# Kernel optimization log

Measured on AMD Instinct MI355X. Metric: run time of the kernel, lower is better.

The kernel has to match this reference:

```python
import jax, jax.numpy as jnp
import numpy as np

NUM_POINTS = 16384
OVERSAMPLE = 3
IMPORTANCE_RATIO = 0.75


def point_sample(feat, coords):
    """grid_sample(bilinear, align_corners=False, zero padding) at [0,1]^2 coords.
    feat: (N, C, H, W); coords: (N, P, 2) with coords[...,0]=x (width), [...,1]=y.
    Returns (N, C, P)."""
    N, C, H, W = feat.shape
    # grid_sample with g = 2c-1, align_corners=False -> pixel = c*size - 0.5
    x = coords[..., 0] * W - 0.5
    y = coords[..., 1] * H - 0.5
    x0 = jnp.floor(x)
    y0 = jnp.floor(y)
    x1 = x0 + 1.0
    y1 = y0 + 1.0
    wx1 = x - x0
    wx0 = 1.0 - wx1
    wy1 = y - y0
    wy0 = 1.0 - wy1
    featf = feat.reshape(N, C, H * W)

    def gather(yi, xi):
        valid = (xi >= 0) & (xi <= W - 1) & (yi >= 0) & (yi <= H - 1)
        xic = jnp.clip(xi, 0, W - 1).astype(jnp.int32)
        yic = jnp.clip(yi, 0, H - 1).astype(jnp.int32)
        idx = yic * W + xic  # (N, P)
        v = jnp.take_along_axis(featf, idx[:, None, :], axis=2)  # (N, C, P)
        return v * valid[:, None, :].astype(feat.dtype)

    out = (gather(y0, x0) * (wy0 * wx0)[:, None, :]
           + gather(y0, x1) * (wy0 * wx1)[:, None, :]
           + gather(y1, x0) * (wy1 * wx0)[:, None, :]
           + gather(y1, x1) * (wy1 * wx1)[:, None, :])
    return out


def calculate_uncertainty(logits):
    """logits: (N, C, P) -> (N, P) uncertainty = top2 - top1 (<= 0)."""
    if logits.shape[1] == 1:
        return -jnp.abs(logits)[:, 0, :]
    top2 = jax.lax.top_k(jnp.moveaxis(logits, 1, -1), 2)[0]  # (N, P, 2)
    return top2[..., 1] - top2[..., 0]


def sample_point_coords(coarse_logits):
    """get_uncertain_point_coords_with_randomness (torch.no_grad branch)."""
    N = coarse_logits.shape[0]
    num_sampled = NUM_POINTS * OVERSAMPLE
    num_imp = int(IMPORTANCE_RATIO * NUM_POINTS)
    num_rand = NUM_POINTS - num_imp
    k1, k2 = jax.random.split(jax.random.key(7))
    cand = jax.random.uniform(k1, (N, num_sampled, 2), dtype=jnp.float32)
    cand_logits = point_sample(coarse_logits, cand)  # (N, C, S)
    unc = calculate_uncertainty(cand_logits)  # (N, S)
    idx = jax.lax.top_k(unc, num_imp)[1]  # (N, num_imp)
    imp = jnp.take_along_axis(cand, idx[..., None], axis=1)  # (N, num_imp, 2)
    rand = jax.random.uniform(k2, (N, num_rand, 2), dtype=jnp.float32)
    return jnp.concatenate([imp, rand], axis=1)  # (N, P, 2)


def point_head(fine, coarse_pts, w0, b0, w1, b1, w2, b2, wp, bp):
    x = jnp.concatenate([fine, coarse_pts], axis=1)  # (N, nin+C, P)
    for w, b in ((w0, b0), (w1, b1), (w2, b2)):
        x = jax.nn.relu(jnp.einsum('oc,ncp->nop', w, x) + b[None, :, None])
        x = jnp.concatenate([x, coarse_pts], axis=1)  # coarse_pred_each_layer
    return jnp.einsum('oc,ncp->nop', wp, x) + bp[None, :, None]  # (N, C, P)


def setup_inputs() -> dict:
    key = jax.random.key(0)
    ks = jax.random.split(key, 8)
    N, C, Hc, Wc = 8, 19, 64, 64
    nin, Hf, Wf = 256, 128, 128
    fin = nin + C  # 275
    return {
        'coarse_sem_seg_logits': jax.random.normal(ks[0], (N, C, Hc, Wc), jnp.float32),
        'features': jax.random.normal(ks[1], (N, nin, Hf, Wf), jnp.float32),
        'w0': jax.random.normal(ks[2], (nin, fin), jnp.float32) * (2.0 / fin) ** 0.5,
        'b0': jnp.zeros((nin,), jnp.float32),
        'w1': jax.random.normal(ks[3], (nin, fin), jnp.float32) * (2.0 / fin) ** 0.5,
        'b1': jnp.zeros((nin,), jnp.float32),
        'w2': jax.random.normal(ks[4], (nin, fin), jnp.float32) * (2.0 / fin) ** 0.5,
        'b2': jnp.zeros((nin,), jnp.float32),
        'wp': jax.random.normal(ks[5], (C, fin), jnp.float32) * 0.001,
        'bp': jnp.zeros((C,), jnp.float32),
    }


def reference(coarse_sem_seg_logits, features, w0, b0, w1, b1, w2, b2, wp, bp):
    # training-mode forward of PointRendSemSegHead
    point_coords = jax.lax.stop_gradient(
        sample_point_coords(jax.lax.stop_gradient(coarse_sem_seg_logits)))
    coarse_pts = point_sample(coarse_sem_seg_logits, point_coords)  # (N, C, P)
    fine_pts = point_sample(features, point_coords)  # (N, nin, P)
    point_logits = point_head(fine_pts, coarse_pts, w0, b0, w1, b1, w2, b2, wp, bp)
    return coarse_sem_seg_logits, point_logits, point_coords
```

## Files before the change

### kernel.cpp

```cpp
#include <hip/hip_runtime.h>
#include <stdint.h>

#pragma clang fp contract(off)

#define NB    8
#define CCH   19
#define FCH   256
#define FIN   275
#define KP    288
#define NPTS  16384
#define NSAMP 49152
#define NIMP  12288
#define NRAND 4096
#define SORT_M 65536
#define CHUNK  8192
#define TP    64
#define XROW  640
#define WBF_OFF (4u << 20)
#define FTR_OFF (8u << 20)
#define FTR_BYTES (134217728ull / 2)

typedef __attribute__((ext_vector_type(8))) short bf16x8;
typedef __attribute__((ext_vector_type(4))) float f32x4;

__host__ __device__ __forceinline__ uint32_t rotl32(uint32_t v, int r) {
  return (v << r) | (v >> (32 - r));
}

__host__ __device__ __forceinline__ void tf2x32(uint32_t k0, uint32_t k1,
                                                uint32_t x0, uint32_t x1,
                                                uint32_t* o0, uint32_t* o1) {
  const uint32_t ks2 = k0 ^ k1 ^ 0x1BD11BDAu;
  x0 += k0; x1 += k1;
#define TF_R(r) { x0 += x1; x1 = rotl32(x1, (r)); x1 ^= x0; }
  TF_R(13) TF_R(15) TF_R(26) TF_R(6)
  x0 += k1;  x1 += ks2 + 1u;
  TF_R(17) TF_R(29) TF_R(16) TF_R(24)
  x0 += ks2; x1 += k0 + 2u;
  TF_R(13) TF_R(15) TF_R(26) TF_R(6)
  x0 += k0;  x1 += k1 + 3u;
  TF_R(17) TF_R(29) TF_R(16) TF_R(24)
  x0 += k1;  x1 += ks2 + 4u;
  TF_R(13) TF_R(15) TF_R(26) TF_R(6)
  x0 += ks2; x1 += k0 + 5u;
#undef TF_R
  *o0 = x0; *o1 = x1;
}

__device__ __forceinline__ float u01_at(uint32_t k0, uint32_t k1, uint32_t i) {
  uint32_t o0, o1;
  tf2x32(k0, k1, 0u, i, &o0, &o1);
  const uint32_t b = o0 ^ o1;
  const float f = __uint_as_float((b >> 9) | 0x3f800000u) - 1.0f;
  return fmaxf(0.0f, f);
}

__device__ __forceinline__ unsigned short f2bf(float f) {
  const uint32_t u = __float_as_uint(f);
  return (unsigned short)((u + 0x7fffu + ((u >> 16) & 1u)) >> 16);
}

__device__ __forceinline__ float bf2f(unsigned short h) {
  return __uint_as_float((uint32_t)h << 16);
}

template <int SZ>
__device__ __forceinline__ void interp(float cx, float cy, int* off, float* wgt) {
  const float X = cx * (float)SZ - 0.5f, Y = cy * (float)SZ - 0.5f;
  const float x0f = floorf(X), y0f = floorf(Y);
  const float fx = X - x0f, fy = Y - y0f;
  const float wx0 = 1.0f - fx, wy0 = 1.0f - fy;
  const int x0 = (int)x0f, y0 = (int)y0f;
  const int x0c = min(max(x0, 0), SZ - 1), x1c = min(max(x0 + 1, 0), SZ - 1);
  const int y0c = min(max(y0, 0), SZ - 1), y1c = min(max(y0 + 1, 0), SZ - 1);
  const bool vx0 = (x0 >= 0) & (x0 <= SZ - 1), vx1 = (x0 >= -1) & (x0 <= SZ - 2);
  const bool vy0 = (y0 >= 0) & (y0 <= SZ - 1), vy1 = (y0 >= -1) & (y0 <= SZ - 2);
  off[0] = y0c * SZ + x0c; wgt[0] = (vy0 & vx0) ? wy0 * wx0 : 0.0f;
  off[1] = y0c * SZ + x1c; wgt[1] = (vy0 & vx1) ? wy0 * fx  : 0.0f;
  off[2] = y1c * SZ + x0c; wgt[2] = (vy1 & vx0) ? fy  * wx0 : 0.0f;
  off[3] = y1c * SZ + x1c; wgt[3] = (vy1 & vx1) ? fy  * fx  : 0.0f;
}

__global__ __launch_bounds__(256) void fusedA(
    const float* __restrict__ feats, unsigned short* __restrict__ ftr,
    const float* __restrict__ coarse, unsigned long long* __restrict__ keys,
    const float* __restrict__ w0, const float* __restrict__ w1,
    const float* __restrict__ w2, const float* __restrict__ wpw,
    unsigned short* __restrict__ wbf, unsigned short* __restrict__ wpb,
    uint32_t k1a, uint32_t k1b, int use_tr) {
  __shared__ unsigned short tile[64][66];
  const int bid = blockIdx.x;
  const int t = threadIdx.x;

  if (bid < 8192) {
    if (!use_tr) return;
    const int nn = bid >> 10;
    const int ct = (bid >> 8) & 3;
    const int pt = bid & 255;
    const int c0 = ct * 64, p0 = pt * 64;
    const float* src = feats + ((size_t)nn << 22);
#pragma unroll 4
    for (int k = 0; k < 16; ++k) {
      const int c = 4 * k + (t >> 6);
      const int p = t & 63;
      tile[p][c] = f2bf(src[((size_t)(c0 + c) << 14) + p0 + p]);
    }
    __syncthreads();
    const int p = t >> 2, q = t & 3;
    const int cb = q * 16;
    uint32_t w[8];
#pragma unroll
    for (int m = 0; m < 8; ++m)
      w[m] = (uint32_t)tile[p][cb + 2 * m] | ((uint32_t)tile[p][cb + 2 * m + 1] << 16);
    unsigned short* dst = ftr + ((((size_t)nn << 14) + p0 + p) << 8) + c0 + cb;
    *(uint4*)(dst)     = make_uint4(w[0], w[1], w[2], w[3]);
    *(uint4*)(dst + 8) = make_uint4(w[4], w[5], w[6], w[7]);
  } else if (bid < 10240) {
    const int tid = (bid - 8192) * 256 + t;
    const int nn = tid >> 16, s = tid & (SORT_M - 1);
    if (s >= NSAMP) { keys[tid] = 0xFFFFFFFFFFFFFFFFull; return; }
    const uint32_t ci = (uint32_t)(((unsigned)nn * NSAMP + (unsigned)s) * 2);
    const float cx = u01_at(k1a, k1b, ci);
    const float cy = u01_at(k1a, k1b, ci + 1);
    const float X = cx * 64.0f - 0.5f, Y = cy * 64.0f - 0.5f;
    const float x0f = floorf(X), y0f = floorf(Y);
    const float fx = X - x0f, fy = Y - y0f;
    const float wx0 = 1.0f - fx, wy0 = 1.0f - fy;
    const int x0 = (int)x0f, y0 = (int)y0f;
    const int x0c = min(max(x0, 0), 63), x1c = min(max(x0 + 1, 0), 63);
    const int y0c = min(max(y0, 0), 63), y1c = min(max(y0 + 1, 0), 63);
    const bool vx0 = (x0 >= 0) & (x0 <= 63), vx1 = (x0 >= -1) & (x0 <= 62);
    const bool vy0 = (y0 >= 0) & (y0 <= 63), vy1 = (y0 >= -1) & (y0 <= 62);
    const float w00 = (vy0 & vx0) ? wy0 * wx0 : 0.0f;
    const float w01 = (vy0 & vx1) ? wy0 * fx  : 0.0f;
    const float w10 = (vy1 & vx0) ? fy  * wx0 : 0.0f;
    const float w11 = (vy1 & vx1) ? fy  * fx  : 0.0f;
    const int o00 = y0c * 64 + x0c, o01 = y0c * 64 + x1c;
    const int o10 = y1c * 64 + x0c, o11 = y1c * 64 + x1c;
    const float* cb = coarse + (size_t)nn * (CCH * 4096);
    float m1 = -3.402823466e38f, m2 = -3.402823466e38f;
    for (int c = 0; c < CCH; ++c) {
      const float* pch = cb + (size_t)c * 4096;
      const float v = ((pch[o00] * w00 + pch[o01] * w01) + pch[o10] * w10) + pch[o11] * w11;
      if (v > m1) { m2 = m1; m1 = v; } else if (v > m2) { m2 = v; }
    }
    const float unc = m2 - m1;
    const uint32_t b = __float_as_uint(unc);
    const uint32_t asc = (b & 0x80000000u) ? ~b : (b | 0x80000000u);
    keys[tid] = ((unsigned long long)(~asc) << 32) | (uint32_t)s;
  } else {
    const int i = (bid - 10240) * 256 + t;
    if (i < 3 * 256 * KP) {
      const int L = i / (256 * KP);
      const int rem = i - L * (256 * KP);
      const int o = rem / KP, k = rem - o * KP;
      const float* W = (L == 0) ? w0 : (L == 1) ? w1 : w2;
      wbf[i] = (k < FIN) ? f2bf(W[o * FIN + k]) : (unsigned short)0;
    } else {
      const int j = i - 3 * 256 * KP;
      const int o = j / KP, k = j - o * KP;
      wpb[j] = (o < CCH && k < FIN) ? f2bf(wpw[o * FIN + k]) : (unsigned short)0;
    }
  }
}

__global__ __launch_bounds__(1024) void bitonic_local(unsigned long long* __restrict__ keys) {
  __shared__ unsigned long long s[CHUNK];
  const int cb = blockIdx.x;
  unsigned long long* a = keys + (size_t)cb * CHUNK;
  const unsigned gbase = (unsigned)(cb * CHUNK) & (SORT_M - 1);
  for (int i = threadIdx.x; i < CHUNK; i += 1024) s[i] = a[i];
  __syncthreads();
  for (int k = 2; k <= CHUNK; k <<= 1) {
    for (int j = k >> 1; j > 0; j >>= 1) {
      for (int pid = threadIdx.x; pid < CHUNK / 2; pid += 1024) {
        const int i = ((pid & ~(j - 1)) << 1) | (pid & (j - 1));
        const int l = i | j;
        const bool up = (((gbase + i) & k) == 0);
        const unsigned long long x = s[i], y = s[l];
        if ((x > y) == up) { s[i] = y; s[l] = x; }
      }
      __syncthreads();
    }
  }
  for (int i = threadIdx.x; i < CHUNK; i += 1024) a[i] = s[i];
}

__global__ __launch_bounds__(256) void bitonic_global(unsigned long long* __restrict__ keys,
                                                      int k, int j) {
  const int t = blockIdx.x * blockDim.x + threadIdx.x;
  const int b = t >> 15, pid = t & 32767;
  const int i = ((pid & ~(j - 1)) << 1) | (pid & (j - 1));
  const int l = i | j;
  const bool up = ((i & k) == 0);
  unsigned long long* a = keys + ((size_t)b << 16);
  const unsigned long long x = a[i], y = a[l];
  if ((x > y) == up) { a[i] = y; a[l] = x; }
}

__global__ __launch_bounds__(1024) void bitonic_finish(unsigned long long* __restrict__ keys,
                                                       int k) {
  __shared__ unsigned long long s[CHUNK];
  const int cb = blockIdx.x;
  unsigned long long* a = keys + (size_t)cb * CHUNK;
  const unsigned gi0 = (unsigned)(cb * CHUNK) & (SORT_M - 1);
  for (int i = threadIdx.x; i < CHUNK; i += 1024) s[i] = a[i];
  __syncthreads();
  const bool up = ((gi0 & k) == 0);
  for (int j = CHUNK >> 1; j > 0; j >>= 1) {
    for (int pid = threadIdx.x; pid < CHUNK / 2; pid += 1024) {
      const int i = ((pid & ~(j - 1)) << 1) | (pid & (j - 1));
      const int l = i | j;
      const unsigned long long x = s[i], y = s[l];
      if ((x > y) == up) { s[i] = y; s[l] = x; }
    }
    __syncthreads();
  }
  for (int i = threadIdx.x; i < CHUNK; i += 1024) a[i] = s[i];
}

__global__ __launch_bounds__(256) void write_coords(const unsigned long long* __restrict__ keys,
                                                    float* __restrict__ outc,
                                                    uint32_t k1a, uint32_t k1b,
                                                    uint32_t k2a, uint32_t k2b) {
  const int t = blockIdx.x * blockDim.x + threadIdx.x;
  if (t >= NB * NPTS) return;
  const int nn = t >> 14, p = t & (NPTS - 1);
  float cx, cy;
  if (p < NIMP) {
    const unsigned idx = (unsigned)(keys[((size_t)nn << 16) + p] & 0xFFFFFFFFu);
    const uint32_t ci = ((unsigned)nn * NSAMP + idx) * 2;
    cx = u01_at(k1a, k1b, ci);
    cy = u01_at(k1a, k1b, ci + 1);
  } else {
    const uint32_t ri = ((unsigned)nn * NRAND + (unsigned)(p - NIMP)) * 2;
    cx = u01_at(k2a, k2b, ri);
    cy = u01_at(k2a, k2b, ri + 1);
  }
  outc[(size_t)t * 2] = cx;
  outc[(size_t)t * 2 + 1] = cy;
}

template <int USE_TR>
__global__ __launch_bounds__(512, 6) void fused_mfma(
    const float* __restrict__ coarse, const float* __restrict__ feats,
    const unsigned short* __restrict__ ftr,
    const float* __restrict__ b0, const float* __restrict__ b1,
    const float* __restrict__ b2, const float* __restrict__ bp,
    const unsigned short* __restrict__ wbf, const unsigned short* __restrict__ wpb,
    const float* __restrict__ pc, float* __restrict__ outl) {
  __shared__ __align__(16) unsigned short xp[TP * (XROW / 2)];

  const int t = threadIdx.x;
  const int nn = blockIdx.x >> 8;
  const int pbase = (blockIdx.x & 255) * TP;

  int offF[4]; float wgtF[4];
  int offC[4]; float wgtC[4];
  int offFc[4]; float wgtFc[4];
  {
    const float2 c = *(const float2*)(pc + ((size_t)nn * NPTS + pbase + (t >> 3)) * 2);
    interp<128>(c.x, c.y, offF, wgtF);
  }
  {
    const float2 c = *(const float2*)(pc + ((size_t)nn * NPTS + pbase + (t & 63)) * 2);
    interp<64>(c.x, c.y, offC, wgtC);
    if (!USE_TR) interp<128>(c.x, c.y, offFc, wgtFc);
  }

  if (USE_TR) {
    const int p = t >> 3, q = t & 7;
    const unsigned short* base = ftr + (((size_t)nn << 14) << 8) + q * 32;
    const unsigned short* n0 = base + ((size_t)offF[0] << 8);
    const unsigned short* n1 = base + ((size_t)offF[1] << 8);
    const unsigned short* n2 = base + ((size_t)offF[2] << 8);
    const unsigned short* n3 = base + ((size_t)offF[3] << 8);
    const float g0 = wgtF[0], g1 = wgtF[1], g2 = wgtF[2], g3 = wgtF[3];
    const unsigned swzp = (unsigned)(p & 7) << 4;
#pragma unroll
    for (int m = 0; m < 4; ++m) {
      const bf16x8 a = *(const bf16x8*)(n0 + m * 8);
      const bf16x8 bq = *(const bf16x8*)(n1 + m * 8);
      const bf16x8 c = *(const bf16x8*)(n2 + m * 8);
      const bf16x8 d = *(const bf16x8*)(n3 + m * 8);
      uint32_t u[4];
#pragma unroll
      for (int e = 0; e < 4; ++e) {
        float v0 = fmaf(bf2f((unsigned short)a[2 * e]), g0,
                   fmaf(bf2f((unsigned short)bq[2 * e]), g1,
                   fmaf(bf2f((unsigned short)c[2 * e]), g2,
                        bf2f((unsigned short)d[2 * e]) * g3)));
        float v1 = fmaf(bf2f((unsigned short)a[2 * e + 1]), g0,
                   fmaf(bf2f((unsigned short)bq[2 * e + 1]), g1,
                   fmaf(bf2f((unsigned short)c[2 * e + 1]), g2,
                        bf2f((unsigned short)d[2 * e + 1]) * g3)));
        u[e] = (uint32_t)f2bf(v0) | ((uint32_t)f2bf(v1) << 16);
      }
      *(uint4*)((char*)xp + p * XROW + (((unsigned)((q * 32 + m * 8) * 2)) ^ swzp)) =
          make_uint4(u[0], u[1], u[2], u[3]);
    }
  }

  for (int i = (USE_TR ? 8192 : 0) + t; i < (KP / 2) * TP; i += 512) {
    const int p = i & (TP - 1);
    const int c0 = (i >> 6) * 2;
    float v0 = 0.0f, v1 = 0.0f;
    if (!USE_TR && c0 < FCH) {
      const float* fb0 = feats + ((size_t)nn << 22) + ((size_t)c0 << 14);
      const float* fb1 = fb0 + 16384;
      v0 = ((fb0[offFc[0]] * wgtFc[0] + fb0[offFc[1]] * wgtFc[1])
           + fb0[offFc[2]] * wgtFc[2]) + fb0[offFc[3]] * wgtFc[3];
      v1 = ((fb1[offFc[0]] * wgtFc[0] + fb1[offFc[1]] * wgtFc[1])
           + fb1[offFc[2]] * wgtFc[2]) + fb1[offFc[3]] * wgtFc[3];
    } else if (c0 >= FCH && c0 < FIN) {
      const float* cb0 = coarse + (size_t)nn * (CCH * 4096) + (size_t)(c0 - FCH) * 4096;
      v0 = ((cb0[offC[0]] * wgtC[0] + cb0[offC[1]] * wgtC[1])
           + cb0[offC[2]] * wgtC[2]) + cb0[offC[3]] * wgtC[3];
      if (c0 + 1 < FIN) {
        const float* cb1 = cb0 + 4096;
        v1 = ((cb1[offC[0]] * wgtC[0] + cb1[offC[1]] * wgtC[1])
             + cb1[offC[2]] * wgtC[2]) + cb1[offC[3]] * wgtC[3];
      }
    }
    const uint32_t u = (uint32_t)f2bf(v0) | ((uint32_t)f2bf(v1) << 16);
    *(uint32_t*)((char*)xp + p * XROW + (((unsigned)(c0 * 2)) ^ ((unsigned)(p & 7) << 4))) = u;
  }

  const int lane = t & 63, wave = t >> 6;
  const int wm = wave & 3, wn = wave >> 2;
  const int l15 = lane & 15, g = lane >> 4;
  const unsigned swz = (unsigned)(l15 & 7) << 4;
  const char* xpB = (const char*)xp;

  const float* Bs[3] = {b0, b1, b2};

  for (int L = 0; L < 3; ++L) {
    __syncthreads();
    const unsigned short* wL = wbf + (size_t)L * (256 * KP);
    const unsigned short* wbase = wL + (size_t)(wm * 64 + l15) * KP + g * 8;

    f32x4 acc[4][2];
#pragma unroll
    for (int mt = 0; mt < 4; ++mt)
#pragma unroll
      for (int nt = 0; nt < 2; ++nt) acc[mt][nt] = (f32x4)(0.0f);

    for (int ks = 0; ks < 9; ++ks) {
      const bf16x8 a0 = *(const bf16x8*)(wbase + 0 * 16 * KP + ks * 32);
      const bf16x8 a1 = *(const bf16x8*)(wbase + 1 * 16 * KP + ks * 32);
      const bf16x8 a2 = *(const bf16x8*)(wbase + 2 * 16 * KP + ks * 32);
      const bf16x8 a3 = *(const bf16x8*)(wbase + 3 * 16 * KP + ks * 32);
      const unsigned kb = (unsigned)(ks * 64 + g * 16) ^ swz;
      const bf16x8 q0 = *(const bf16x8*)(xpB + (wn * 32 + 0 + l15) * XROW + kb);
      const bf16x8 q1 = *(const bf16x8*)(xpB + (wn * 32 + 16 + l15) * XROW + kb);
      acc[0][0] = __builtin_amdgcn_mfma_f32_16x16x32_bf16(a0, q0, acc[0][0], 0, 0, 0);
      acc[1][0] = __builtin_amdgcn_mfma_f32_16x16x32_bf16(a1, q0, acc[1][0], 0, 0, 0);
      acc[2][0] = __builtin_amdgcn_mfma_f32_16x16x32_bf16(a2, q0, acc[2][0], 0, 0, 0);
      acc[3][0] = __builtin_amdgcn_mfma_f32_16x16x32_bf16(a3, q0, acc[3][0], 0, 0, 0);
      acc[0][1] = __builtin_amdgcn_mfma_f32_16x16x32_bf16(a0, q1, acc[0][1], 0, 0, 0);
      acc[1][1] = __builtin_amdgcn_mfma_f32_16x16x32_bf16(a1, q1, acc[1][1], 0, 0, 0);
      acc[2][1] = __builtin_amdgcn_mfma_f32_16x16x32_bf16(a2, q1, acc[2][1], 0, 0, 0);
      acc[3][1] = __builtin_amdgcn_mfma_f32_16x16x32_bf16(a3, q1, acc[3][1], 0, 0, 0);
    }
    __syncthreads();

    const float* __restrict__ Bv = Bs[L];
#pragma unroll
    for (int mt = 0; mt < 4; ++mt) {
      const int ch0 = wm * 64 + mt * 16 + (g << 2);
      const float4 bv = *(const float4*)(Bv + ch0);
#pragma unroll
      for (int nt = 0; nt < 2; ++nt) {
        const int p = wn * 32 + nt * 16 + l15;
        const f32x4 v = acc[mt][nt];
        const unsigned short h0 = f2bf(fmaxf(v[0] + bv.x, 0.0f));
        const unsigned short h1 = f2bf(fmaxf(v[1] + bv.y, 0.0f));
        const unsigned short h2 = f2bf(fmaxf(v[2] + bv.z, 0.0f));
        const unsigned short h3 = f2bf(fmaxf(v[3] + bv.w, 0.0f));
        uint2 u;
        u.x = (uint32_t)h0 | ((uint32_t)h1 << 16);
        u.y = (uint32_t)h2 | ((uint32_t)h3 << 16);
        *(uint2*)((char*)xp + p * XROW + (((unsigned)(ch0 * 2)) ^ swz)) = u;
      }
    }
  }
  __syncthreads();

  const int hmt = wave >> 2, hnt = wave & 3;
  const unsigned short* hbase = wpb + (size_t)(hmt * 16 + l15) * KP + g * 8;
  f32x4 hacc = (f32x4)(0.0f);
  for (int ks = 0; ks < 9; ++ks) {
    const unsigned kb = (unsigned)(ks * 64 + g * 16) ^ swz;
    const bf16x8 ha = *(const bf16x8*)(hbase + ks * 32);
    const bf16x8 hb = *(const bf16x8*)(xpB + (hnt * 16 + l15) * XROW + kb);
    hacc = __builtin_amdgcn_mfma_f32_16x16x32_bf16(ha, hb, hacc, 0, 0, 0);
  }
  const int p = pbase + hnt * 16 + l15;
#pragma unroll
  for (int j = 0; j < 4; ++j) {
    const int ch = hmt * 16 + (g << 2) + j;
    if (ch < CCH)
      outl[((size_t)nn * CCH + ch) * NPTS + p] = hacc[j] + bp[ch];
  }
}

extern "C" void kernel_launch(void* const* d_in, const int* in_sizes, int n_in,
                              void* d_out, int out_size, void* d_ws, size_t ws_size,
                              hipStream_t stream) {
  const float* coarse = (const float*)d_in[0];
  const float* feats  = (const float*)d_in[1];
  const float* w0 = (const float*)d_in[2]; const float* b0 = (const float*)d_in[3];
  const float* w1 = (const float*)d_in[4]; const float* b1 = (const float*)d_in[5];
  const float* w2 = (const float*)d_in[6]; const float* b2 = (const float*)d_in[7];
  const float* wp = (const float*)d_in[8]; const float* bp = (const float*)d_in[9];

  float* out0 = (float*)d_out;
  float* outL = out0 + 622592;
  float* outC = outL + 2490368;

  unsigned long long* keys = (unsigned long long*)d_ws;
  unsigned short* wbf = (unsigned short*)((char*)d_ws + WBF_OFF);
  unsigned short* wpb = wbf + 3 * 256 * KP;
  unsigned short* ftr = (unsigned short*)((char*)d_ws + FTR_OFF);
  const int use_tr = (ws_size >= (size_t)FTR_OFF + FTR_BYTES) ? 1 : 0;

  uint32_t k1a, k1b, k2a, k2b;
  tf2x32(0u, 7u, 0u, 0u, &k1a, &k1b);
  tf2x32(0u, 7u, 0u, 1u, &k2a, &k2b);

  hipMemcpyAsync(out0, coarse, 622592 * sizeof(float),
                 hipMemcpyDeviceToDevice, stream);

  fusedA<<<11140, 256, 0, stream>>>(feats, ftr, coarse, keys,
                                    w0, w1, w2, wp, wbf, wpb, k1a, k1b, use_tr);

  bitonic_local<<<64, 1024, 0, stream>>>(keys);
  bitonic_global<<<1024, 256, 0, stream>>>(keys, 16384, 8192);
  bitonic_finish<<<64, 1024, 0, stream>>>(keys, 16384);
  bitonic_global<<<1024, 256, 0, stream>>>(keys, 32768, 16384);
  bitonic_global<<<1024, 256, 0, stream>>>(keys, 32768, 8192);
  bitonic_finish<<<64, 1024, 0, stream>>>(keys, 32768);
  bitonic_global<<<1024, 256, 0, stream>>>(keys, 65536, 32768);
  bitonic_global<<<1024, 256, 0, stream>>>(keys, 65536, 16384);
  bitonic_global<<<1024, 256, 0, stream>>>(keys, 65536, 8192);
  bitonic_finish<<<64, 1024, 0, stream>>>(keys, 65536);

  write_coords<<<512, 256, 0, stream>>>(keys, outC, k1a, k1b, k2a, k2b);

  if (use_tr)
    fused_mfma<1><<<2048, 512, 0, stream>>>(coarse, feats, ftr, b0, b1, b2, bp,
                                            wbf, wpb, outC, outL);
  else
    fused_mfma<0><<<2048, 512, 0, stream>>>(coarse, feats, ftr, b0, b1, b2, bp,
                                            wbf, wpb, outC, outL);
}
```

Before: 408.2 us.

## Sort only needed top chunks in final bitonic stage and fuse coord writing

In the last bitonic merge stage, the later global passes and the final local pass now only process the lower portion of each row, since only the top NIMP keys (the first 12288 entries) are consumed. The final in-shared-memory merge is fused with the coordinate generation into a single kernel with 16 blocks, which removes the separate write_coords launch. The MLP kernel's occupancy hint is lowered from 6 to 4 and its layer loop is unrolled with a direct bias-pointer select. The fused final kernel runs only 16 blocks, which leaves most of the GPU idle during that step.

New measurement: 389.3 us. -4.6%, faster.

```diff
diff --git a/kernel.cpp b/kernel.cpp
--- a/kernel.cpp
+++ b/kernel.cpp
@@ -187,9 +187,9 @@
 }
 
 __global__ __launch_bounds__(256) void bitonic_global(unsigned long long* __restrict__ keys,
-                                                      int k, int j) {
+                                                      int k, int j, int ppb_shift) {
   const int t = blockIdx.x * blockDim.x + threadIdx.x;
-  const int b = t >> 15, pid = t & 32767;
+  const int b = t >> ppb_shift, pid = t & ((1 << ppb_shift) - 1);
   const int i = ((pid & ~(j - 1)) << 1) | (pid & (j - 1));
   const int l = i | j;
   const bool up = ((i & k) == 0);
@@ -219,30 +219,44 @@
   for (int i = threadIdx.x; i < CHUNK; i += 1024) a[i] = s[i];
 }
 
-__global__ __launch_bounds__(256) void write_coords(const unsigned long long* __restrict__ keys,
-                                                    float* __restrict__ outc,
-                                                    uint32_t k1a, uint32_t k1b,
-                                                    uint32_t k2a, uint32_t k2b) {
-  const int t = blockIdx.x * blockDim.x + threadIdx.x;
-  if (t >= NB * NPTS) return;
-  const int nn = t >> 14, p = t & (NPTS - 1);
-  float cx, cy;
-  if (p < NIMP) {
-    const unsigned idx = (unsigned)(keys[((size_t)nn << 16) + p] & 0xFFFFFFFFu);
-    const uint32_t ci = ((unsigned)nn * NSAMP + idx) * 2;
-    cx = u01_at(k1a, k1b, ci);
-    cy = u01_at(k1a, k1b, ci + 1);
-  } else {
-    const uint32_t ri = ((unsigned)nn * NRAND + (unsigned)(p - NIMP)) * 2;
-    cx = u01_at(k2a, k2b, ri);
-    cy = u01_at(k2a, k2b, ri + 1);
-  }
-  outc[(size_t)t * 2] = cx;
-  outc[(size_t)t * 2 + 1] = cy;
+__global__ __launch_bounds__(1024) void finlow_coords(
+    const unsigned long long* __restrict__ keys, float* __restrict__ outc,
+    uint32_t k1a, uint32_t k1b, uint32_t k2a, uint32_t k2b) {
+  __shared__ unsigned long long s[CHUNK];
+  const int nn = blockIdx.x >> 1, half = blockIdx.x & 1;
+  const unsigned long long* a = keys + ((size_t)nn << 16) + half * CHUNK;
+  for (int i = threadIdx.x; i < CHUNK; i += 1024) s[i] = a[i];
+  __syncthreads();
+  for (int j = CHUNK >> 1; j > 0; j >>= 1) {
+    for (int pid = threadIdx.x; pid < CHUNK / 2; pid += 1024) {
+      const int i = ((pid & ~(j - 1)) << 1) | (pid & (j - 1));
+      const int l = i | j;
+      const unsigned long long x = s[i], y = s[l];
+      if (x > y) { s[i] = y; s[l] = x; }
+    }
+    __syncthreads();
+  }
+  const int pb = half * CHUNK;
+  for (int q = threadIdx.x; q < CHUNK; q += 1024) {
+    const int p = pb + q;
+    float cx, cy;
+    if (p < NIMP) {
+      const unsigned idx = (unsigned)(s[q] & 0xFFFFFFFFu);
+      const uint32_t ci = ((unsigned)nn * NSAMP + idx) * 2;
+      cx = u01_at(k1a, k1b, ci);
+      cy = u01_at(k1a, k1b, ci + 1);
+    } else {
+      const uint32_t ri = ((unsigned)nn * NRAND + (unsigned)(p - NIMP)) * 2;
+      cx = u01_at(k2a, k2b, ri);
+      cy = u01_at(k2a, k2b, ri + 1);
+    }
+    float* o = outc + (((size_t)nn << 14) + p) * 2;
+    o[0] = cx; o[1] = cy;
+  }
 }
 
 template <int USE_TR>
-__global__ __launch_bounds__(512, 6) void fused_mfma(
+__global__ __launch_bounds__(512, 4) void fused_mfma(
     const float* __restrict__ coarse, const float* __restrict__ feats,
     const unsigned short* __restrict__ ftr,
     const float* __restrict__ b0, const float* __restrict__ b1,
@@ -332,10 +346,10 @@
   const unsigned swz = (unsigned)(l15 & 7) << 4;
   const char* xpB = (const char*)xp;
 
-  const float* Bs[3] = {b0, b1, b2};
-
+#pragma unroll
   for (int L = 0; L < 3; ++L) {
     __syncthreads();
+    const float* Bv = (L == 0) ? b0 : (L == 1) ? b1 : b2;
     const unsigned short* wL = wbf + (size_t)L * (256 * KP);
     const unsigned short* wbase = wL + (size_t)(wm * 64 + l15) * KP + g * 8;
 
@@ -364,7 +378,6 @@
     }
     __syncthreads();
 
-    const float* __restrict__ Bv = Bs[L];
 #pragma unroll
     for (int mt = 0; mt < 4; ++mt) {
       const int ch0 = wm * 64 + mt * 16 + (g << 2);
@@ -435,17 +448,15 @@
                                     w0, w1, w2, wp, wbf, wpb, k1a, k1b, use_tr);
 
   bitonic_local<<<64, 1024, 0, stream>>>(keys);
-  bitonic_global<<<1024, 256, 0, stream>>>(keys, 16384, 8192);
+  bitonic_global<<<1024, 256, 0, stream>>>(keys, 16384, 8192, 15);
   bitonic_finish<<<64, 1024, 0, stream>>>(keys, 16384);
-  bitonic_global<<<1024, 256, 0, stream>>>(keys, 32768, 16384);
-  bitonic_global<<<1024, 256, 0, stream>>>(keys, 32768, 8192);
+  bitonic_global<<<1024, 256, 0, stream>>>(keys, 32768, 16384, 15);
+  bitonic_global<<<1024, 256, 0, stream>>>(keys, 32768, 8192, 15);
   bitonic_finish<<<64, 1024, 0, stream>>>(keys, 32768);
-  bitonic_global<<<1024, 256, 0, stream>>>(keys, 65536, 32768);
-  bitonic_global<<<1024, 256, 0, stream>>>(keys, 65536, 16384);
-  bitonic_global<<<1024, 256, 0, stream>>>(keys, 65536, 8192);
-  bitonic_finish<<<64, 1024, 0, stream>>>(keys, 65536);
-
-  write_coords<<<512, 256, 0, stream>>>(keys, outC, k1a, k1b, k2a, k2b);
+  bitonic_global<<<1024, 256, 0, stream>>>(keys, 65536, 32768, 15);
+  bitonic_global<<<512, 256, 0, stream>>>(keys, 65536, 16384, 14);
+  bitonic_global<<<256, 256, 0, stream>>>(keys, 65536, 8192, 13);
+  finlow_coords<<<16, 1024, 0, stream>>>(keys, outC, k1a, k1b, k2a, k2b);
 
   if (use_tr)
     fused_mfma<1><<<2048, 512, 0, stream>>>(coarse, feats, ftr, b0, b1, b2, bp,
```
